# Kernel tuning notes

Hardware: AMD Instinct MI355X
Metric: run time of the kernel (lower is better)

## Reference

```python
import jax, jax.numpy as jnp
import numpy as np

EMBED = 768
HEADS = 12
HEAD_DIM = EMBED // HEADS
HIDDEN = 4 * EMBED
EPS = 1e-5


def layernorm(x, gamma, beta):
    mu = jnp.mean(x, axis=-1, keepdims=True)
    var = jnp.var(x, axis=-1, keepdims=True)
    return (x - mu) * jax.lax.rsqrt(var + EPS) * gamma + beta


def setup_inputs() -> dict:
    key = jax.random.key(0)
    ks = jax.random.split(key, 16)
    s = 0.02
    return {
        "x": jax.random.normal(ks[0], (4, 2048, EMBED), jnp.float32),
        "w_qkv": jax.random.normal(ks[1], (EMBED, 3 * EMBED), jnp.float32) * s,
        "b_qkv": jnp.zeros((3 * EMBED,), jnp.float32),
        "w_proj": jax.random.normal(ks[2], (EMBED, EMBED), jnp.float32) * s,
        "b_proj": jnp.zeros((EMBED,), jnp.float32),
        "w_fc1": jax.random.normal(ks[3], (EMBED, HIDDEN), jnp.float32) * s,
        "b_fc1": jnp.zeros((HIDDEN,), jnp.float32),
        "w_fc2": jax.random.normal(ks[4], (HIDDEN, EMBED), jnp.float32) * s,
        "b_fc2": jnp.zeros((EMBED,), jnp.float32),
        "gamma1": jnp.ones((EMBED,), jnp.float32),
        "beta1": jnp.zeros((EMBED,), jnp.float32),
        "gamma2": jnp.ones((EMBED,), jnp.float32),
        "beta2": jnp.zeros((EMBED,), jnp.float32),
    }


def reference(x, w_qkv, b_qkv, w_proj, b_proj, w_fc1, b_fc1, w_fc2, b_fc2,
              gamma1, beta1, gamma2, beta2):
    B, N, E = x.shape
    # --- pre-norm self-attention (dropout = identity at eval) ---
    h = layernorm(x, gamma1, beta1)
    qkv = (h @ w_qkv + b_qkv).reshape(B, N, 3, HEADS, HEAD_DIM)
    q, k, v = qkv[:, :, 0], qkv[:, :, 1], qkv[:, :, 2]  # [B,N,H,D]
    scale = 1.0 / np.sqrt(HEAD_DIM).astype(np.float32)
    scores = jnp.einsum('bnhd,bmhd->bhnm', q, k) * scale  # [B,H,N,N]
    probs = jax.nn.softmax(scores, axis=-1)
    attended = jnp.einsum('bhnm,bmhd->bnhd', probs, v).reshape(B, N, E)
    x = x + attended @ w_proj + b_proj
    # --- pre-norm MLP with exact GELU ---
    h = layernorm(x, gamma2, beta2)
    h = jax.nn.gelu(h @ w_fc1 + b_fc1, approximate=False)
    x = x + h @ w_fc2 + b_fc2
    return x
```

## Files before the change

kernel.cpp:

```cpp
#include <hip/hip_runtime.h>
#include <hip/hip_bf16.h>
#include <math.h>

typedef __attribute__((ext_vector_type(8))) short bf16x8;
typedef __attribute__((ext_vector_type(4))) float f32x4;
typedef __attribute__((ext_vector_type(4))) short s16x4;

__device__ __forceinline__ void gload16(const void* g, void* l) {
  __builtin_amdgcn_global_load_lds((const __attribute__((address_space(1))) void*)g,
                                   (__attribute__((address_space(3))) void*)l, 16, 0, 0);
}

__device__ __forceinline__ short f2bf(float f) {
  unsigned int x = __builtin_bit_cast(unsigned int, f);
  x += 0x7fffu + ((x >> 16) & 1u);
  return (short)(x >> 16);
}

__device__ __forceinline__ unsigned int pkbf_rn(float a, float b) {
  unsigned int ua = __builtin_bit_cast(unsigned int, a) + 0x8000u;
  unsigned int ub = __builtin_bit_cast(unsigned int, b) + 0x8000u;
  return __builtin_amdgcn_perm(ub, ua, 0x07060302u);
}

__device__ __forceinline__ f32x4 mfma16(bf16x8 a, bf16x8 b, f32x4 c) {
  return __builtin_amdgcn_mfma_f32_16x16x32_bf16(a, b, c, 0, 0, 0);
}

__device__ __forceinline__ void l2map(int bid, int MB, int NB, int& bm, int& bn) {
  int xcd = bid & 7;
  int i = bid >> 3;
  int MB8 = MB >> 3;
  int S = (MB8 < 4) ? MB8 : 4;
  int sub = i / (NB * S);
  int r2 = i - sub * (NB * S);
  bn = r2 / S;
  int bmi = r2 - bn * S;
  bm = xcd * MB8 + sub * S + bmi;
}

__global__ __launch_bounds__(256) void ln_kernel(
    const float* __restrict__ x, const float* __restrict__ gamma,
    const float* __restrict__ beta, short* __restrict__ out)
{
  int row = blockIdx.x * 4 + (threadIdx.x >> 6);
  int lane = threadIdx.x & 63;
  const float* xr = x + (size_t)row * 768;
  float4 v[3];
  v[0] = *(const float4*)(xr + lane * 4);
  v[1] = *(const float4*)(xr + 256 + lane * 4);
  v[2] = *(const float4*)(xr + 512 + lane * 4);
  float s = 0.f, ss = 0.f;
  for (int i = 0; i < 3; i++) {
    s  += v[i].x + v[i].y + v[i].z + v[i].w;
    ss += v[i].x*v[i].x + v[i].y*v[i].y + v[i].z*v[i].z + v[i].w*v[i].w;
  }
  for (int m = 32; m >= 1; m >>= 1) { s += __shfl_xor(s, m); ss += __shfl_xor(ss, m); }
  float mu = s * (1.f/768.f);
  float var = ss * (1.f/768.f) - mu*mu;
  float rs = rsqrtf(var + 1e-5f);
  short* orow = out + (size_t)row * 768;
  for (int i = 0; i < 3; i++) {
    int c = i*256 + lane*4;
    float4 g = *(const float4*)(gamma + c);
    float4 b = *(const float4*)(beta + c);
    s16x4 o;
    o.x = f2bf((v[i].x - mu)*rs*g.x + b.x);
    o.y = f2bf((v[i].y - mu)*rs*g.y + b.y);
    o.z = f2bf((v[i].z - mu)*rs*g.z + b.z);
    o.w = f2bf((v[i].w - mu)*rs*g.w + b.w);
    *(s16x4*)(orow + c) = o;
  }
}

__device__ __forceinline__ void tcvt_tile(
    const float* __restrict__ in, short* __restrict__ out, int K, int N, int bid)
{
  __shared__ float tile[64][65];
  int nb = N >> 6;
  int bk = bid / nb, bn = bid % nb;
  int tx = threadIdx.x & 63, ty = threadIdx.x >> 6;
  int k0 = bk << 6, n0 = bn << 6;
  for (int i = 0; i < 16; i++) {
    int r = i*4 + ty;
    tile[r][tx] = in[(size_t)(k0 + r) * N + n0 + tx];
  }
  __syncthreads();
  for (int i = 0; i < 16; i++) {
    int r = i*4 + ty;
    out[(size_t)(n0 + r) * K + k0 + tx] = f2bf(tile[tx][r]);
  }
}

__global__ __launch_bounds__(256) void transpose_all(
    const float* __restrict__ wqkv, const float* __restrict__ wproj,
    const float* __restrict__ wfc1, const float* __restrict__ wfc2,
    short* __restrict__ oqkv, short* __restrict__ oproj,
    short* __restrict__ ofc1, short* __restrict__ ofc2)
{
  int bid = blockIdx.x;
  if (bid < 432)       tcvt_tile(wqkv, oqkv, 768, 2304, bid);
  else if (bid < 576)  tcvt_tile(wproj, oproj, 768, 768, bid - 432);
  else if (bid < 1152) tcvt_tile(wfc1, ofc1, 768, 3072, bid - 576);
  else                 tcvt_tile(wfc2, ofc2, 3072, 768, bid - 1152);
}

template<int EPI, int TAG>
__global__ __launch_bounds__(256, 4) void gemm4(
    const short* __restrict__ A, const short* __restrict__ BT,
    const float* __restrict__ bias, const float* __restrict__ res,
    void* __restrict__ outp, void* __restrict__ outp2, int M, int N, int K)
{
  __shared__ short As[128*64];
  __shared__ short Bs[128*64];
  int MB = M >> 7, NB = N >> 7;
  int bm, bn;
  l2map(blockIdx.x, MB, NB, bm, bn);
  int t = threadIdx.x;
  int lane = t & 63, lr = lane & 15, lg = lane >> 4;
  int wave = t >> 6, wm = wave >> 1, wn = wave & 1;
  int ur = t >> 3;
  int sw8 = ((t & 7) ^ (ur & 7)) * 8;

  const short* Abase = A  + (size_t)(bm*128 + ur) * K + sw8;
  const short* Bbase = BT + (size_t)(bn*128 + ur) * K + sw8;

  f32x4 acc[4][4] = {};
  int nt = K >> 6;

  for (int tt = 0; tt < nt; ++tt) {
    __syncthreads();
    #pragma unroll
    for (int i = 0; i < 4; i++) gload16(Abase + (size_t)i*32*K + tt*64, As + i*2048 + t*8);
    #pragma unroll
    for (int i = 0; i < 4; i++) gload16(Bbase + (size_t)i*32*K + tt*64, Bs + i*2048 + t*8);
    __syncthreads();
    #pragma unroll
    for (int kf = 0; kf < 2; kf++) {
      int ck = (((kf<<2) + lg) ^ (lr & 7)) << 3;
      bf16x8 af[4], bf[4];
      #pragma unroll
      for (int m=0;m<4;m++) af[m] = *(const bf16x8*)(As + (wm*64 + m*16 + lr)*64 + ck);
      #pragma unroll
      for (int n=0;n<4;n++) bf[n] = *(const bf16x8*)(Bs + (wn*64 + n*16 + lr)*64 + ck);
      #pragma unroll
      for (int m=0;m<4;m++)
        #pragma unroll
        for (int n=0;n<4;n++)
          acc[m][n] = mfma16(af[m], bf[n], acc[m][n]);
    }
  }

  int rowb = bm*128 + wm*64;
  int colb = bn*128 + wn*64;
  if (EPI == 3 && colb >= 1536) {
    short* vT = (short*)outp2;
    #pragma unroll
    for (int mf=0; mf<4; mf++) {
      int row0 = rowb + mf*16 + lg*4;
      int bbatch = row0 >> 11;
      int tok = row0 & 2047;
      #pragma unroll
      for (int nf=0; nf<4; nf++) {
        int col = colb + nf*16 + lr;
        int vcol = col - 1536;
        float bv = bias[col];
        s16x4 o;
        #pragma unroll
        for (int r=0;r<4;r++) o[r] = f2bf(acc[mf][nf][r] + bv);
        *(s16x4*)(vT + ((size_t)(bbatch*12 + (vcol>>6))*64 + (vcol&63))*2048 + tok) = o;
      }
    }
  } else {
    float osc = (EPI == 3 && colb < 768) ? 0.1803368801111244f : 1.0f;
    #pragma unroll
    for (int mf=0; mf<4; mf++) {
      #pragma unroll
      for (int nf=0; nf<4; nf++) {
        int col = colb + nf*16 + lr;
        float bv = bias[col];
        #pragma unroll
        for (int r=0;r<4;r++) {
          int row = rowb + mf*16 + lg*4 + r;
          float vv = acc[mf][nf][r] + bv;
          if (EPI == 3) {
            ((short*)outp)[(size_t)row * 1536 + col] = f2bf(vv * osc);
          } else if (EPI == 1) {
            float u = vv * (0.7978845608f + 0.0356774081f * vv * vv);
            float e = __expf(2.f * u);
            float th = 1.f - 2.f / (e + 1.f);
            vv = 0.5f * vv * (1.f + th);
            ((short*)outp)[(size_t)row * N + col] = f2bf(vv);
          } else {
            size_t idx = (size_t)row * N + col;
            ((float*)outp)[idx] = vv + res[idx];
          }
        }
      }
    }
  }
}

__global__ __launch_bounds__(256, 4) void attn_kernel(
    const short* __restrict__ qk, const short* __restrict__ vT, short* __restrict__ out)
{
  __shared__ short Ks[64*64];
  __shared__ short Vs[64*64];
  __shared__ short Ps[4][32*72];
  int bh = blockIdx.x >> 4, qt = blockIdx.x & 15;
  int b = bh / 12, h = bh % 12;
  int t = threadIdx.x, wave = t >> 6, lane = t & 63, lr = lane & 15, lg = lane >> 4;
  size_t tok0 = (size_t)b * 2048;

  const short* qb = qk + (tok0 + qt*128 + wave*32) * 1536 + h*64;
  bf16x8 aq[2][2];
  for (int m=0;m<2;m++)
    for (int kf=0;kf<2;kf++)
      aq[m][kf] = *(const bf16x8*)(qb + (size_t)(m*16 + lr)*1536 + kf*32 + lg*8);

  bf16x8 ones;
  #pragma unroll
  for (int j=0;j<8;j++) ones[j] = (short)0x3F80;

  f32x4 accO[2][4] = {};
  f32x4 accL[2] = {};

  int rd = t >> 3;
  int ksw = ((t&7) ^ (rd&7)) * 8;
  int ktok = 4*(rd & 15) + (rd >> 4);
  const short* kg = qk + (tok0 + ktok)*1536 + 768 + h*64 + ksw;
  const short* vg = vT + ((size_t)bh*64 + rd)*2048 + ksw;
  short* Psw = &Ps[wave][0];

  int ck0 = ((lg ^ (lr&7)) << 3);
  int ck1 = (((4+lg) ^ (lr&7)) << 3);

  for (int kt = 0; kt < 32; kt++) {
    __syncthreads();
    gload16(kg + (size_t)kt*64*1536,              Ks + wave*512);
    gload16(kg + (size_t)(kt*64 + 2)*1536,        Ks + wave*512 + 2048);
    gload16(vg + kt*64,                            Vs + wave*512);
    gload16(vg + (size_t)32*2048 + kt*64,          Vs + wave*512 + 2048);
    __syncthreads();

    f32x4 s[2][4] = {};
    __builtin_amdgcn_s_setprio(1);
    for (int kf=0;kf<2;kf++) {
      int ck = kf ? ck1 : ck0;
      for (int n=0;n<4;n++) {
        int row = n*16 + lr;
        bf16x8 bk = *(const bf16x8*)(Ks + row*64 + ck);
        s[0][n] = mfma16(aq[0][kf], bk, s[0][n]);
        s[1][n] = mfma16(aq[1][kf], bk, s[1][n]);
      }
    }
    __builtin_amdgcn_s_setprio(0);

    #pragma unroll
    for (int m=0;m<2;m++)
      #pragma unroll
      for (int r=0;r<4;r++) {
        float p0 = __builtin_amdgcn_exp2f(s[m][0][r]);
        float p1 = __builtin_amdgcn_exp2f(s[m][1][r]);
        float p2 = __builtin_amdgcn_exp2f(s[m][2][r]);
        float p3 = __builtin_amdgcn_exp2f(s[m][3][r]);
        uint2 pk;
        pk.x = pkbf_rn(p0, p1);
        pk.y = pkbf_rn(p2, p3);
        *(uint2*)(Psw + (m*16 + lg*4 + r)*72 + lr*4) = pk;
      }

    __builtin_amdgcn_s_setprio(1);
    for (int kf=0;kf<2;kf++) {
      int ck = kf ? ck1 : ck0;
      bf16x8 ap0 = *(const bf16x8*)(Psw + lr*72 + kf*32 + lg*8);
      bf16x8 ap1 = *(const bf16x8*)(Psw + (16+lr)*72 + kf*32 + lg*8);
      accL[0] = mfma16(ap0, ones, accL[0]);
      accL[1] = mfma16(ap1, ones, accL[1]);
      for (int df=0;df<4;df++) {
        int row = df*16 + lr;
        bf16x8 bv = *(const bf16x8*)(Vs + row*64 + ck);
        accO[0][df] = mfma16(ap0, bv, accO[0][df]);
        accO[1][df] = mfma16(ap1, bv, accO[1][df]);
      }
    }
    __builtin_amdgcn_s_setprio(0);
  }

  size_t row0 = tok0 + qt*128 + wave*32;
  for (int m=0;m<2;m++) {
    f32x4 rcp;
    #pragma unroll
    for (int r=0;r<4;r++) rcp[r] = 1.0f / accL[m][r];
    for (int df=0;df<4;df++)
      #pragma unroll
      for (int r=0;r<4;r++) {
        float o = accO[m][df][r] * rcp[r];
        out[(row0 + m*16 + lg*4 + r)*768 + h*64 + df*16 + lr] = f2bf(o);
      }
  }
}

extern "C" void kernel_launch(void* const* d_in, const int* in_sizes, int n_in,
                              void* d_out, int out_size, void* d_ws, size_t ws_size,
                              hipStream_t stream) {
  const float* x      = (const float*)d_in[0];
  const float* w_qkv  = (const float*)d_in[1];
  const float* b_qkv  = (const float*)d_in[2];
  const float* w_proj = (const float*)d_in[3];
  const float* b_proj = (const float*)d_in[4];
  const float* w_fc1  = (const float*)d_in[5];
  const float* b_fc1  = (const float*)d_in[6];
  const float* w_fc2  = (const float*)d_in[7];
  const float* b_fc2  = (const float*)d_in[8];
  const float* gamma1 = (const float*)d_in[9];
  const float* beta1  = (const float*)d_in[10];
  const float* gamma2 = (const float*)d_in[11];
  const float* beta2  = (const float*)d_in[12];

  char* ws = (char*)d_ws;
  short* wqkvT = (short*)ws;  ws += (size_t)2304*768*2;
  short* wprojT = (short*)ws; ws += (size_t)768*768*2;
  short* wfc1T = (short*)ws;  ws += (size_t)3072*768*2;
  short* wfc2T = (short*)ws;  ws += (size_t)768*3072*2;
  short* hbuf = (short*)ws;   ws += (size_t)8192*768*2;
  short* qkbuf = (short*)ws;  ws += (size_t)8192*1536*2;
  short* vTbuf = (short*)ws;  ws += (size_t)48*64*2048*2;
  short* attn = (short*)ws;   ws += (size_t)8192*768*2;
  float* x2 = (float*)ws;     ws += (size_t)8192*768*4;
  short* gbuf = (short*)ws;   ws += (size_t)8192*3072*2;

  transpose_all<<<1728, 256, 0, stream>>>(w_qkv, w_proj, w_fc1, w_fc2,
                                          wqkvT, wprojT, wfc1T, wfc2T);

  ln_kernel<<<2048, 256, 0, stream>>>(x, gamma1, beta1, hbuf);
  gemm4<3,0><<<1152, 256, 0, stream>>>(hbuf, wqkvT, b_qkv, nullptr, qkbuf, vTbuf, 8192, 2304, 768);
  attn_kernel<<<48*16, 256, 0, stream>>>(qkbuf, vTbuf, attn);
  gemm4<2,1><<<384, 256, 0, stream>>>(attn, wprojT, b_proj, x, x2, nullptr, 8192, 768, 768);
  ln_kernel<<<2048, 256, 0, stream>>>(x2, gamma2, beta2, hbuf);
  gemm4<1,2><<<1536, 256, 0, stream>>>(hbuf, wfc1T, b_fc1, nullptr, gbuf, nullptr, 8192, 3072, 768);
  gemm4<2,3><<<384, 256, 0, stream>>>(gbuf, wfc2T, b_fc2, x2, d_out, nullptr, 8192, 768, 3072);
}
```

Before: 262.6 us.

## Halve attention query tile per block to double grid size and occupancy

The attention kernel now gives each wave 16 query rows instead of 32, so a block covers 64 queries and the grid grows from 768 to 1536 blocks. Launch bounds rise to 6 blocks per CU and the P scratch buffer shrinks. This aims to fill more of the GPU's CUs and hide latency with more resident waves. The cost is that each K/V tile loaded into LDS is reused by half as many queries, doubling global K/V traffic and the number of syncs per unit of work.

```diff
diff --git a/kernel.cpp b/kernel.cpp
--- a/kernel.cpp
+++ b/kernel.cpp
@@ -201,29 +201,28 @@
   }
 }
 
-__global__ __launch_bounds__(256, 4) void attn_kernel(
+__global__ __launch_bounds__(256, 6) void attn_kernel(
     const short* __restrict__ qk, const short* __restrict__ vT, short* __restrict__ out)
 {
   __shared__ short Ks[64*64];
   __shared__ short Vs[64*64];
-  __shared__ short Ps[4][32*72];
-  int bh = blockIdx.x >> 4, qt = blockIdx.x & 15;
+  __shared__ short Ps[4][16*72];
+  int bh = blockIdx.x >> 5, qt = blockIdx.x & 31;
   int b = bh / 12, h = bh % 12;
   int t = threadIdx.x, wave = t >> 6, lane = t & 63, lr = lane & 15, lg = lane >> 4;
   size_t tok0 = (size_t)b * 2048;
 
-  const short* qb = qk + (tok0 + qt*128 + wave*32) * 1536 + h*64;
-  bf16x8 aq[2][2];
-  for (int m=0;m<2;m++)
-    for (int kf=0;kf<2;kf++)
-      aq[m][kf] = *(const bf16x8*)(qb + (size_t)(m*16 + lr)*1536 + kf*32 + lg*8);
+  const short* qb = qk + (tok0 + qt*64 + wave*16) * 1536 + h*64;
+  bf16x8 aq[2];
+  for (int kf=0;kf<2;kf++)
+    aq[kf] = *(const bf16x8*)(qb + (size_t)lr*1536 + kf*32 + lg*8);
 
   bf16x8 ones;
   #pragma unroll
   for (int j=0;j<8;j++) ones[j] = (short)0x3F80;
 
-  f32x4 accO[2][4] = {};
-  f32x4 accL[2] = {};
+  f32x4 accO[4] = {};
+  f32x4 accL = {};
 
   int rd = t >> 3;
   int ksw = ((t&7) ^ (rd&7)) * 8;
@@ -243,62 +242,55 @@
     gload16(vg + (size_t)32*2048 + kt*64,          Vs + wave*512 + 2048);
     __syncthreads();
 
-    f32x4 s[2][4] = {};
+    f32x4 s[4] = {};
     __builtin_amdgcn_s_setprio(1);
     for (int kf=0;kf<2;kf++) {
       int ck = kf ? ck1 : ck0;
+      bf16x8 a = aq[kf];
+      #pragma unroll
       for (int n=0;n<4;n++) {
-        int row = n*16 + lr;
-        bf16x8 bk = *(const bf16x8*)(Ks + row*64 + ck);
-        s[0][n] = mfma16(aq[0][kf], bk, s[0][n]);
-        s[1][n] = mfma16(aq[1][kf], bk, s[1][n]);
+        bf16x8 bk = *(const bf16x8*)(Ks + (n*16+lr)*64 + ck);
+        s[n] = mfma16(a, bk, s[n]);
       }
     }
     __builtin_amdgcn_s_setprio(0);
 
     #pragma unroll
-    for (int m=0;m<2;m++)
-      #pragma unroll
-      for (int r=0;r<4;r++) {
-        float p0 = __builtin_amdgcn_exp2f(s[m][0][r]);
-        float p1 = __builtin_amdgcn_exp2f(s[m][1][r]);
-        float p2 = __builtin_amdgcn_exp2f(s[m][2][r]);
-        float p3 = __builtin_amdgcn_exp2f(s[m][3][r]);
-        uint2 pk;
-        pk.x = pkbf_rn(p0, p1);
-        pk.y = pkbf_rn(p2, p3);
-        *(uint2*)(Psw + (m*16 + lg*4 + r)*72 + lr*4) = pk;
-      }
+    for (int r=0;r<4;r++) {
+      float p0 = __builtin_amdgcn_exp2f(s[0][r]);
+      float p1 = __builtin_amdgcn_exp2f(s[1][r]);
+      float p2 = __builtin_amdgcn_exp2f(s[2][r]);
+      float p3 = __builtin_amdgcn_exp2f(s[3][r]);
+      uint2 pk;
+      pk.x = pkbf_rn(p0, p1);
+      pk.y = pkbf_rn(p2, p3);
+      *(uint2*)(Psw + (lg*4 + r)*72 + lr*4) = pk;
+    }
 
     __builtin_amdgcn_s_setprio(1);
     for (int kf=0;kf<2;kf++) {
       int ck = kf ? ck1 : ck0;
-      bf16x8 ap0 = *(const bf16x8*)(Psw + lr*72 + kf*32 + lg*8);
-      bf16x8 ap1 = *(const bf16x8*)(Psw + (16+lr)*72 + kf*32 + lg*8);
-      accL[0] = mfma16(ap0, ones, accL[0]);
-      accL[1] = mfma16(ap1, ones, accL[1]);
+      bf16x8 ap = *(const bf16x8*)(Psw + lr*72 + kf*32 + lg*8);
+      accL = mfma16(ap, ones, accL);
+      #pragma unroll
       for (int df=0;df<4;df++) {
-        int row = df*16 + lr;
-        bf16x8 bv = *(const bf16x8*)(Vs + row*64 + ck);
-        accO[0][df] = mfma16(ap0, bv, accO[0][df]);
-        accO[1][df] = mfma16(ap1, bv, accO[1][df]);
+        bf16x8 bv = *(const bf16x8*)(Vs + (df*16+lr)*64 + ck);
+        accO[df] = mfma16(ap, bv, accO[df]);
       }
     }
     __builtin_amdgcn_s_setprio(0);
   }
 
-  size_t row0 = tok0 + qt*128 + wave*32;
-  for (int m=0;m<2;m++) {
-    f32x4 rcp;
-    #pragma unroll
-    for (int r=0;r<4;r++) rcp[r] = 1.0f / accL[m][r];
-    for (int df=0;df<4;df++)
-      #pragma unroll
-      for (int r=0;r<4;r++) {
-        float o = accO[m][df][r] * rcp[r];
-        out[(row0 + m*16 + lg*4 + r)*768 + h*64 + df*16 + lr] = f2bf(o);
-      }
-  }
+  size_t row0 = tok0 + qt*64 + wave*16;
+  f32x4 rcp;
+  #pragma unroll
+  for (int r=0;r<4;r++) rcp[r] = 1.0f / accL[r];
+  for (int df=0;df<4;df++)
+    #pragma unroll
+    for (int r=0;r<4;r++) {
+      float o = accO[df][r] * rcp[r];
+      out[(row0 + lg*4 + r)*768 + h*64 + df*16 + lr] = f2bf(o);
+    }
 }
 
 extern "C" void kernel_launch(void* const* d_in, const int* in_sizes, int n_in,
@@ -335,7 +327,7 @@
 
   ln_kernel<<<2048, 256, 0, stream>>>(x, gamma1, beta1, hbuf);
   gemm4<3,0><<<1152, 256, 0, stream>>>(hbuf, wqkvT, b_qkv, nullptr, qkbuf, vTbuf, 8192, 2304, 768);
-  attn_kernel<<<48*16, 256, 0, stream>>>(qkbuf, vTbuf, attn);
+  attn_kernel<<<48*32, 256, 0, stream>>>(qkbuf, vTbuf, attn);
   gemm4<2,1><<<384, 256, 0, stream>>>(attn, wprojT, b_proj, x, x2, nullptr, 8192, 768, 768);
   ln_kernel<<<2048, 256, 0, stream>>>(x2, gamma2, beta2, hbuf);
   gemm4<1,2><<<1536, 256, 0, stream>>>(hbuf, wfc1T, b_fc1, nullptr, gbuf, nullptr, 8192, 3072, 768);
```

Measured after the change: 270.7 us. 1.03x slower.
